# Kernel tuning notes

Measured on AMD Instinct MI355X. Metric: run time of the kernel, lower is better.

Reference implementation:

```python
import jax, jax.numpy as jnp
import numpy as np

E, B = 4, 16384
STATE, ACT, HID = 29, 8, 512
N_POSE, N_LEG = 13, 16

def _leg_inputs(state, act=None):
    # gather per-leg features: for each leg i (stride-2 over 8 joints)
    # [pos_a, vel_a, pos_b, vel_b, (act_a, act_b)] -> concat legs along batch dim
    leg = state[..., -N_LEG:]
    blocks = []
    for i in range(0, 8, 2):
        feats = [leg[..., i], leg[..., 8 + i], leg[..., i + 1], leg[..., 8 + i + 1]]
        if act is not None:
            feats += [act[..., i], act[..., i + 1]]
        blocks.append(jnp.stack(feats, axis=2))
    return jnp.concatenate(blocks, axis=1)  # [E, 4B, 4 or 6]

def _mlp(x, w0, b0, w1, b1, w2, b2, mu, sigma):
    x = (x - mu) / (sigma + 1e-8)
    x = jax.nn.relu(jnp.einsum('ebi,eih->ebh', x, w0) + b0)
    x = jax.nn.relu(jnp.einsum('ebh,ehk->ebk', x, w1) + b1)
    return jnp.einsum('ebh,eho->ebo', x, w2) + b2

def _leg_format(next_legs, b):
    # vectorized form of the original nested-loop scatter in leg_predict
    e = next_legs.shape[0]
    c = next_legs.reshape(e, 4, b, 4).transpose(0, 2, 1, 3)  # [E,B,leg,comp]
    first = jnp.stack([c[..., 0], c[..., 2]], axis=-1).reshape(e, b, 8)   # pos block
    second = jnp.stack([c[..., 1], c[..., 3]], axis=-1).reshape(e, b, 8)  # vel block
    zeros = jnp.zeros((e, b, N_POSE), next_legs.dtype)
    return jnp.concatenate([zeros, first, second], axis=-1)  # [E,B,29]

def reference(state, act, wl0, bl0, wl1, bl1, wl2, bl2, wp0, bp0, wp1, bp1, wp2, bp2,
              mu_leg, sigma_leg, mu_pose, sigma_pose,
              mu_t_leg, sigma_t_leg, mu_t_pose, sigma_t_pose):
    b = state.shape[1]
    out = _mlp(_leg_inputs(state, act), wl0, bl0, wl1, bl1, wl2, bl2, mu_leg, sigma_leg)
    legs_diff = out[..., :4] * (sigma_t_leg + 1e-8) + mu_t_leg          # [E,4B,4] mean head
    legs_curr = _leg_inputs(state)                                       # [E,4B,4]
    next_state_legs = _leg_format(legs_curr + legs_diff, b)              # [E,B,29]
    legs_diff_fmt = _leg_format(legs_diff, b)[..., -N_LEG:]              # [E,B,16]
    pose_in = jnp.concatenate([state[..., :N_POSE], legs_diff_fmt], axis=-1)  # [E,B,29]
    pose = _mlp(pose_in, wp0, bp0, wp1, bp1, wp2, bp2, mu_pose, sigma_pose)[..., :N_POSE]
    pose = pose * (sigma_t_pose + 1e-8) + mu_t_pose + state[..., :N_POSE]
    next_state = jnp.concatenate([pose, next_state_legs[..., N_POSE:]], axis=-1)
    return next_state.mean(0)  # [B, 29]

def setup_inputs():
    key = jax.random.key(0)
    ks = jax.random.split(key, 10)
    s = 0.05
    return {
        'state': jax.random.normal(ks[0], (E, B, STATE), jnp.float32),
        'act': jax.random.normal(ks[1], (E, B, ACT), jnp.float32),
        'wl0': jax.random.normal(ks[2], (E, 6, HID), jnp.float32) * s,
        'bl0': jnp.zeros((E, 1, HID), jnp.float32),
        'wl1': jax.random.normal(ks[3], (E, HID, HID), jnp.float32) * s,
        'bl1': jnp.zeros((E, 1, HID), jnp.float32),
        'wl2': jax.random.normal(ks[4], (E, HID, 8), jnp.float32) * s,
        'bl2': jnp.zeros((E, 1, 8), jnp.float32),
        'wp0': jax.random.normal(ks[5], (E, STATE, HID), jnp.float32) * s,
        'bp0': jnp.zeros((E, 1, HID), jnp.float32),
        'wp1': jax.random.normal(ks[6], (E, HID, HID), jnp.float32) * s,
        'bp1': jnp.zeros((E, 1, HID), jnp.float32),
        'wp2': jax.random.normal(ks[7], (E, HID, 2 * N_POSE), jnp.float32) * s,
        'bp2': jnp.zeros((E, 1, 2 * N_POSE), jnp.float32),
        'mu_leg': jnp.zeros((1, 6), jnp.float32),
        'sigma_leg': jnp.ones((1, 6), jnp.float32),
        'mu_pose': jnp.zeros((1, STATE), jnp.float32),
        'sigma_pose': jnp.ones((1, STATE), jnp.float32),
        'mu_t_leg': jnp.zeros((1, 4), jnp.float32),
        'sigma_t_leg': jnp.ones((1, 4), jnp.float32),
        'mu_t_pose': jnp.zeros((1, N_POSE), jnp.float32),
        'sigma_t_pose': jnp.ones((1, N_POSE), jnp.float32),
    }
```

## Files before the change

### kernel.cpp

```cpp
#include <hip/hip_runtime.h>


#define E_ 4
#define B_ 16384
#define H1S 520
#define H2S 136
#define A0S 40

typedef float f32x4 __attribute__((ext_vector_type(4)));
typedef __bf16 bf16x8 __attribute__((ext_vector_type(8)));

__device__ __forceinline__ f32x4 mfma16(bf16x8 a, bf16x8 b, f32x4 c) {
  return __builtin_amdgcn_mfma_f32_16x16x32_bf16(a, b, c, 0, 0, 0);
}

__device__ __forceinline__ void fmt_map(int k, int& ib, int& j) {
  if (k < 8) { ib = k >> 1; j = (k & 1) ? 2 : 0; }
  else { int k8 = k - 8; ib = k8 >> 1; j = (k8 & 1) ? 3 : 1; }
}

__device__ __forceinline__ void pack_one(int idx, int per_e, int KT, int Kreal,
                                         int Nsrc, int Nval,
                                         const float* __restrict__ src,
                                         const float* __restrict__ sigma,
                                         __bf16* __restrict__ dst)
{
  int e = idx / per_e;
  int rem = idx - e * per_e;
  int g = rem >> 9;
  int nt = g / KT;
  int kt = g - nt * KT;
  int li = rem & 511;
  int lane = li >> 3, j = li & 7;
  int k = kt * 32 + (lane >> 4) * 8 + j;
  int n = nt * 16 + (lane & 15);
  float v = 0.f;
  if (k < Kreal && n < Nval) {
    v = src[(size_t)e * Kreal * Nsrc + (size_t)k * Nsrc + n];
    if (sigma) v *= 1.f / (sigma[k] + 1e-8f);
  }
  dst[idx] = (__bf16)v;
}

__global__ void prep_kernel(const float* __restrict__ wl0, const float* __restrict__ wl1,
                            const float* __restrict__ wl2, const float* __restrict__ wp0,
                            const float* __restrict__ wp1, const float* __restrict__ wp2,
                            const float* __restrict__ bl0, const float* __restrict__ bp0,
                            const float* __restrict__ mu_leg, const float* __restrict__ sigma_leg,
                            const float* __restrict__ mu_pose, const float* __restrict__ sigma_pose,
                            __bf16* __restrict__ WL0p, __bf16* __restrict__ WL1p,
                            __bf16* __restrict__ WL2p, __bf16* __restrict__ WP0p,
                            __bf16* __restrict__ WP1p, __bf16* __restrict__ WP2p,
                            float* __restrict__ bl0f, float* __restrict__ bp0f)
{
  const int S0 = 65536, S1 = 1048576, S2 = 32768;
  const int total = 2 * (S0 + S1 + S2) + 4096;
  for (int idx0 = blockIdx.x * blockDim.x + threadIdx.x; idx0 < total;
       idx0 += gridDim.x * blockDim.x) {
    int x = idx0;
    if (x < S0)              { pack_one(x, 16384, 1, 6, 512, 512, wl0, sigma_leg, WL0p); }
    else if ((x -= S0) < S1) { pack_one(x, 262144, 16, 512, 512, 512, wl1, nullptr, WL1p); }
    else if ((x -= S1) < S2) { pack_one(x, 8192, 16, 512, 8, 8, wl2, nullptr, WL2p); }
    else if ((x -= S2) < S0) { pack_one(x, 16384, 1, 29, 512, 512, wp0, sigma_pose, WP0p); }
    else if ((x -= S0) < S1) { pack_one(x, 262144, 16, 512, 512, 512, wp1, nullptr, WP1p); }
    else if ((x -= S1) < S2) { pack_one(x, 8192, 16, 512, 26, 16, wp2, nullptr, WP2p); }
    else {
      x -= S2;
      if (x < 2048) {
        int e = x >> 9, n = x & 511;
        float s = bl0[e * 512 + n];
        #pragma unroll
        for (int k = 0; k < 6; ++k)
          s -= mu_leg[k] / (sigma_leg[k] + 1e-8f) * wl0[(e * 6 + k) * 512 + n];
        bl0f[e * 512 + n] = s;
      } else {
        x -= 2048;
        int e = x >> 9, n = x & 511;
        float s = bp0[e * 512 + n];
        for (int k = 0; k < 29; ++k)
          s -= mu_pose[k] / (sigma_pose[k] + 1e-8f) * wp0[(e * 29 + k) * 512 + n];
        bp0f[e * 512 + n] = s;
      }
    }
  }
}

__global__ __launch_bounds__(512) void fused_kernel(
    const float* __restrict__ state, const float* __restrict__ act,
    const float* __restrict__ bl1, const float* __restrict__ bl2,
    const float* __restrict__ bp1, const float* __restrict__ bp2,
    const float* __restrict__ mu_t_leg, const float* __restrict__ sigma_t_leg,
    const float* __restrict__ mu_t_pose, const float* __restrict__ sigma_t_pose,
    const __bf16* __restrict__ WL0p, const __bf16* __restrict__ WL1p,
    const __bf16* __restrict__ WL2p, const __bf16* __restrict__ WP0p,
    const __bf16* __restrict__ WP1p, const __bf16* __restrict__ WP2p,
    const float* __restrict__ bl0f, const float* __restrict__ bp0f,
    float* __restrict__ out)
{
  __shared__ alignas(16) __bf16 h1[128 * H1S];
  __shared__ alignas(16) __bf16 h2c[64 * H2S];
  __shared__ float ldiff[64][16];
  __shared__ float legacc[64][16];
  __bf16* a0s = h2c;

  const int tid = threadIdx.x;
  const int wv = tid >> 6;
  const int lane = tid & 63;
  const int quad = lane >> 4;
  const int l16 = lane & 15;
  const int b0 = blockIdx.x * 64;

  for (int i = tid; i < 64 * 16; i += 512) ((float*)legacc)[i] = 0.f;
  f32x4 posacc = {0.f, 0.f, 0.f, 0.f};
  __syncthreads();

  for (int e = 0; e < E_; ++e) {
    const float* se = state + (size_t)e * B_ * 29;
    const float* ae = act + (size_t)e * B_ * 8;

    for (int half = 0; half < 2; ++half) {
      __syncthreads();
      for (int i = tid; i < 128 * 32; i += 512) {
        int r = i >> 5, c = i & 31;
        float v = 0.f;
        if (c < 6) {
          int ib = r >> 5;
          int b = b0 + half * 32 + (r & 31);
          const float* sp = se + (size_t)b * 29;
          if (c == 0) v = sp[13 + 2 * ib];
          else if (c == 1) v = sp[21 + 2 * ib];
          else if (c == 2) v = sp[14 + 2 * ib];
          else if (c == 3) v = sp[22 + 2 * ib];
          else if (c == 4) v = ae[(size_t)b * 8 + 2 * ib];
          else v = ae[(size_t)b * 8 + 2 * ib + 1];
        }
        a0s[r * A0S + c] = (__bf16)v;
      }
      __syncthreads();

      {
        const __bf16* W0 = WL0p + (size_t)e * 16384;
        const float* b0v = bl0f + e * 512;
        bf16x8 bfr[4]; float bs[4];
        #pragma unroll
        for (int i = 0; i < 4; ++i) {
          int ct = wv * 4 + i;
          bfr[i] = *(const bf16x8*)(W0 + ((size_t)ct * 64 + lane) * 8);
          bs[i] = b0v[ct * 16 + l16];
        }
        for (int rt = 0; rt < 8; ++rt) {
          bf16x8 afr = *(const bf16x8*)&a0s[(rt * 16 + l16) * A0S + quad * 8];
          #pragma unroll
          for (int i = 0; i < 4; ++i) {
            f32x4 acc = {bs[i], bs[i], bs[i], bs[i]};
            acc = mfma16(afr, bfr[i], acc);
            int col = (wv * 4 + i) * 16 + l16;
            #pragma unroll
            for (int r = 0; r < 4; ++r)
              h1[(rt * 16 + quad * 4 + r) * H1S + col] = (__bf16)fmaxf(acc[r], 0.f);
          }
        }
      }
      __syncthreads();

      const __bf16* W1 = WL1p + (size_t)e * 262144;
      const __bf16* W2 = WL2p + (size_t)e * 8192;
      const float* b1v = bl1 + e * 512;
      const int rg = wv >> 2, cg = wv & 3;
      float bv2 = (l16 < 8) ? bl2[e * 8 + l16] : 0.f;
      f32x4 oacc = {bv2, bv2, bv2, bv2};

      for (int cc = 0; cc < 4; ++cc) {
        f32x4 acc[4][2];
        #pragma unroll
        for (int ct = 0; ct < 2; ++ct) {
          float bias = b1v[cc * 128 + cg * 32 + ct * 16 + l16];
          #pragma unroll
          for (int i = 0; i < 4; ++i) acc[i][ct] = (f32x4){bias, bias, bias, bias};
        }
        const __bf16* Wc = W1 + (size_t)(cc * 8 + cg * 2) * 8192;
        #pragma unroll 4
        for (int kt = 0; kt < 16; ++kt) {
          bf16x8 afr[4];
          #pragma unroll
          for (int i = 0; i < 4; ++i)
            afr[i] = *(const bf16x8*)&h1[(rg * 64 + i * 16 + l16) * H1S + kt * 32 + quad * 8];
          #pragma unroll
          for (int ct = 0; ct < 2; ++ct) {
            bf16x8 bfr = *(const bf16x8*)(Wc + (((size_t)ct * 16 + kt) * 64 + lane) * 8);
            #pragma unroll
            for (int i = 0; i < 4; ++i) acc[i][ct] = mfma16(afr[i], bfr, acc[i][ct]);
          }
        }
        #pragma unroll
        for (int hh = 0; hh < 2; ++hh) {
          __syncthreads();
          if (rg == hh) {
            #pragma unroll
            for (int i = 0; i < 4; ++i)
              #pragma unroll
              for (int ct = 0; ct < 2; ++ct)
                #pragma unroll
                for (int r = 0; r < 4; ++r)
                  h2c[(i * 16 + quad * 4 + r) * H2S + cg * 32 + ct * 16 + l16] =
                      (__bf16)fmaxf(acc[i][ct][r], 0.f);
          }
          __syncthreads();
          if ((wv >> 2) == hh) {
            #pragma unroll
            for (int k2 = 0; k2 < 4; ++k2) {
              bf16x8 afr2 = *(const bf16x8*)&h2c[((wv & 3) * 16 + l16) * H2S + k2 * 32 + quad * 8];
              bf16x8 bfr2 = *(const bf16x8*)(W2 + ((size_t)(cc * 4 + k2) * 64 + lane) * 8);
              oacc = mfma16(afr2, bfr2, oacc);
            }
          }
        }
      }
      if (l16 < 4) {
        float sc = sigma_t_leg[l16] + 1e-8f;
        float mv = mu_t_leg[l16];
        #pragma unroll
        for (int r = 0; r < 4; ++r) {
          int L = wv * 16 + quad * 4 + r;
          ldiff[half * 32 + (L & 31)][(L >> 5) * 4 + l16] = oacc[r] * sc + mv;
        }
      }
    }

    __syncthreads();
    for (int i = tid; i < 64 * 32; i += 512) {
      int t = i >> 5, c = i & 31;
      float v = 0.f;
      if (c < 13) v = se[(size_t)(b0 + t) * 29 + c];
      else if (c < 29) { int ib, j; fmt_map(c - 13, ib, j); v = ldiff[t][ib * 4 + j]; }
      a0s[t * A0S + c] = (__bf16)v;
    }
    for (int i = tid; i < 64 * 16; i += 512) {
      int t = i >> 4, k = i & 15;
      int ib, j; fmt_map(k, ib, j);
      legacc[t][k] += se[(size_t)(b0 + t) * 29 + 13 + k] + ldiff[t][ib * 4 + j];
    }
    __syncthreads();

    {
      const __bf16* W0 = WP0p + (size_t)e * 16384;
      const float* b0v = bp0f + e * 512;
      bf16x8 bfr[4]; float bs[4];
      #pragma unroll
      for (int i = 0; i < 4; ++i) {
        int ct = wv * 4 + i;
        bfr[i] = *(const bf16x8*)(W0 + ((size_t)ct * 64 + lane) * 8);
        bs[i] = b0v[ct * 16 + l16];
      }
      for (int rt = 0; rt < 4; ++rt) {
        bf16x8 afr = *(const bf16x8*)&a0s[(rt * 16 + l16) * A0S + quad * 8];
        #pragma unroll
        for (int i = 0; i < 4; ++i) {
          f32x4 acc = {bs[i], bs[i], bs[i], bs[i]};
          acc = mfma16(afr, bfr[i], acc);
          int col = (wv * 4 + i) * 16 + l16;
          #pragma unroll
          for (int r = 0; r < 4; ++r)
            h1[(rt * 16 + quad * 4 + r) * H1S + col] = (__bf16)fmaxf(acc[r], 0.f);
        }
      }
    }
    __syncthreads();

    {
      const __bf16* W1 = WP1p + (size_t)e * 262144;
      const __bf16* W2 = WP2p + (size_t)e * 8192;
      const float* b1v = bp1 + e * 512;
      float bvp = bp2[e * 26 + l16];
      f32x4 po = {bvp, bvp, bvp, bvp};

      for (int cc2 = 0; cc2 < 2; ++cc2) {
        f32x4 acc[4][2];
        #pragma unroll
        for (int ct = 0; ct < 2; ++ct) {
          float bias = b1v[cc2 * 256 + wv * 32 + ct * 16 + l16];
          #pragma unroll
          for (int i = 0; i < 4; ++i) acc[i][ct] = (f32x4){bias, bias, bias, bias};
        }
        const __bf16* Wc = W1 + (size_t)(cc2 * 16 + wv * 2) * 8192;
        #pragma unroll 4
        for (int kt = 0; kt < 16; ++kt) {
          bf16x8 afr[4];
          #pragma unroll
          for (int i = 0; i < 4; ++i)
            afr[i] = *(const bf16x8*)&h1[(i * 16 + l16) * H1S + kt * 32 + quad * 8];
          #pragma unroll
          for (int ct = 0; ct < 2; ++ct) {
            bf16x8 bfr = *(const bf16x8*)(Wc + (((size_t)ct * 16 + kt) * 64 + lane) * 8);
            #pragma unroll
            for (int i = 0; i < 4; ++i) acc[i][ct] = mfma16(afr[i], bfr, acc[i][ct]);
          }
        }
        #pragma unroll
        for (int hh = 0; hh < 2; ++hh) {
          __syncthreads();
          if ((wv >> 2) == hh) {
            int cgl = wv & 3;
            #pragma unroll
            for (int i = 0; i < 4; ++i)
              #pragma unroll
              for (int ct = 0; ct < 2; ++ct)
                #pragma unroll
                for (int r = 0; r < 4; ++r)
                  h2c[(i * 16 + quad * 4 + r) * H2S + cgl * 32 + ct * 16 + l16] =
                      (__bf16)fmaxf(acc[i][ct][r], 0.f);
          }
          __syncthreads();
          if (wv < 4) {
            #pragma unroll
            for (int k2 = 0; k2 < 4; ++k2) {
              bf16x8 afr2 = *(const bf16x8*)&h2c[(wv * 16 + l16) * H2S + k2 * 32 + quad * 8];
              bf16x8 bfr2 = *(const bf16x8*)(W2 + ((size_t)(cc2 * 8 + hh * 4 + k2) * 64 + lane) * 8);
              po = mfma16(afr2, bfr2, po);
            }
          }
        }
      }
      if (wv < 4 && l16 < 13) {
        float sc = sigma_t_pose[l16] + 1e-8f;
        float mv = mu_t_pose[l16];
        #pragma unroll
        for (int r = 0; r < 4; ++r) {
          int row = wv * 16 + quad * 4 + r;
          posacc[r] += po[r] * sc + mv + se[(size_t)(b0 + row) * 29 + l16];
        }
      }
    }
  }

  if (wv < 4 && l16 < 13) {
    #pragma unroll
    for (int r = 0; r < 4; ++r) {
      int row = wv * 16 + quad * 4 + r;
      out[(size_t)(b0 + row) * 29 + l16] = 0.25f * posacc[r];
    }
  }
  for (int i = tid; i < 64 * 16; i += 512) {
    int t = i >> 4, k = i & 15;
    out[(size_t)(b0 + t) * 29 + 13 + k] = 0.25f * legacc[t][k];
  }
}

extern "C" void kernel_launch(void* const* d_in, const int* in_sizes, int n_in,
                              void* d_out, int out_size, void* d_ws, size_t ws_size,
                              hipStream_t stream) {
  const float* state = (const float*)d_in[0];
  const float* act = (const float*)d_in[1];
  const float* wl0 = (const float*)d_in[2];
  const float* bl0 = (const float*)d_in[3];
  const float* wl1 = (const float*)d_in[4];
  const float* bl1 = (const float*)d_in[5];
  const float* wl2 = (const float*)d_in[6];
  const float* bl2 = (const float*)d_in[7];
  const float* wp0 = (const float*)d_in[8];
  const float* bp0 = (const float*)d_in[9];
  const float* wp1 = (const float*)d_in[10];
  const float* bp1 = (const float*)d_in[11];
  const float* wp2 = (const float*)d_in[12];
  const float* bp2 = (const float*)d_in[13];
  const float* mu_leg = (const float*)d_in[14];
  const float* sigma_leg = (const float*)d_in[15];
  const float* mu_pose = (const float*)d_in[16];
  const float* sigma_pose = (const float*)d_in[17];
  const float* mu_t_leg = (const float*)d_in[18];
  const float* sigma_t_leg = (const float*)d_in[19];
  const float* mu_t_pose = (const float*)d_in[20];
  const float* sigma_t_pose = (const float*)d_in[21];
  float* out = (float*)d_out;

  char* ws = (char*)d_ws;
  __bf16* WL0p = (__bf16*)(ws);
  __bf16* WL1p = (__bf16*)(ws + 131072);
  __bf16* WL2p = (__bf16*)(ws + 2228224);
  __bf16* WP0p = (__bf16*)(ws + 2293760);
  __bf16* WP1p = (__bf16*)(ws + 2424832);
  __bf16* WP2p = (__bf16*)(ws + 4521984);
  float* bl0f = (float*)(ws + 4587520);
  float* bp0f = (float*)(ws + 4595712);

  prep_kernel<<<512, 256, 0, stream>>>(wl0, wl1, wl2, wp0, wp1, wp2, bl0, bp0,
                                       mu_leg, sigma_leg, mu_pose, sigma_pose,
                                       WL0p, WL1p, WL2p, WP0p, WP1p, WP2p,
                                       bl0f, bp0f);
  fused_kernel<<<256, 512, 0, stream>>>(state, act, bl1, bl2, bp1, bp2,
                                        mu_t_leg, sigma_t_leg, mu_t_pose, sigma_t_pose,
                                        WL0p, WL1p, WL2p, WP0p, WP1p, WP2p,
                                        bl0f, bp0f, out);
}
```

Baseline: 375.7 us.

## Halve block tile to 32 rows, 256 threads, XOR-swizzled LDS without padding

Each block now handles 32 batch rows with 4 waves instead of 64 rows with 8 waves, and the grid doubles to 512 blocks. Launch bounds ask for two blocks per CU so more work is resident. Padded LDS strides give way to an XOR swizzle on the h1/h2 buffers, which shrinks LDS use while still avoiding bank conflicts. Leg accumulators move into registers, and the pose-head partial sums are reduced across waves through LDS. The cost is that each block reloads the weights for half as many rows, so weight traffic per row doubles, and there are more barriers.

```diff
diff --git a/kernel.cpp b/kernel.cpp
--- a/kernel.cpp
+++ b/kernel.cpp
@@ -3,15 +3,19 @@
 
 #define E_ 4
 #define B_ 16384
-#define H1S 520
-#define H2S 136
-#define A0S 40
 
 typedef float f32x4 __attribute__((ext_vector_type(4)));
 typedef __bf16 bf16x8 __attribute__((ext_vector_type(8)));
 
 __device__ __forceinline__ f32x4 mfma16(bf16x8 a, bf16x8 b, f32x4 c) {
   return __builtin_amdgcn_mfma_f32_16x16x32_bf16(a, b, c, 0, 0, 0);
+}
+
+__device__ __forceinline__ __bf16* swz_ptr(__bf16* base, int row, int col,
+                                           int rowshift) {
+  int byte = (row << rowshift) + (col << 1);
+  byte ^= (row & 7) << 4;
+  return (__bf16*)((char*)base + byte);
 }
 
 __device__ __forceinline__ void fmt_map(int k, int& ib, int& j) {
@@ -85,7 +89,7 @@
   }
 }
 
-__global__ __launch_bounds__(512) void fused_kernel(
+__global__ __launch_bounds__(256, 2) void fused_kernel(
     const float* __restrict__ state, const float* __restrict__ act,
     const float* __restrict__ bl1, const float* __restrict__ bl2,
     const float* __restrict__ bp1, const float* __restrict__ bp2,
@@ -97,10 +101,9 @@
     const float* __restrict__ bl0f, const float* __restrict__ bp0f,
     float* __restrict__ out)
 {
-  __shared__ alignas(16) __bf16 h1[128 * H1S];
-  __shared__ alignas(16) __bf16 h2c[64 * H2S];
-  __shared__ float ldiff[64][16];
-  __shared__ float legacc[64][16];
+  __shared__ alignas(16) __bf16 h1[64 * 512];
+  __shared__ alignas(16) __bf16 h2c[64 * 64];
+  __shared__ float ldiff[32][16];
   __bf16* a0s = h2c;
 
   const int tid = threadIdx.x;
@@ -108,56 +111,56 @@
   const int lane = tid & 63;
   const int quad = lane >> 4;
   const int l16 = lane & 15;
-  const int b0 = blockIdx.x * 64;
-
-  for (int i = tid; i < 64 * 16; i += 512) ((float*)legacc)[i] = 0.f;
+  const int b0 = blockIdx.x * 32;
+
+  const int lt = tid >> 3;
+  const int lk = tid & 7;
+  float legacc0 = 0.f, legacc1 = 0.f;
   f32x4 posacc = {0.f, 0.f, 0.f, 0.f};
-  __syncthreads();
 
   for (int e = 0; e < E_; ++e) {
     const float* se = state + (size_t)e * B_ * 29;
     const float* ae = act + (size_t)e * B_ * 8;
 
-    for (int half = 0; half < 2; ++half) {
+    for (int h = 0; h < 2; ++h) {
       __syncthreads();
-      for (int i = tid; i < 128 * 32; i += 512) {
+      for (int i = tid; i < 64 * 32; i += 256) {
         int r = i >> 5, c = i & 31;
+        int ib = h * 2 + (r >> 5);
+        int b = b0 + (r & 31);
+        const float* sp = se + (size_t)b * 29;
         float v = 0.f;
-        if (c < 6) {
-          int ib = r >> 5;
-          int b = b0 + half * 32 + (r & 31);
-          const float* sp = se + (size_t)b * 29;
-          if (c == 0) v = sp[13 + 2 * ib];
-          else if (c == 1) v = sp[21 + 2 * ib];
-          else if (c == 2) v = sp[14 + 2 * ib];
-          else if (c == 3) v = sp[22 + 2 * ib];
-          else if (c == 4) v = ae[(size_t)b * 8 + 2 * ib];
-          else v = ae[(size_t)b * 8 + 2 * ib + 1];
-        }
-        a0s[r * A0S + c] = (__bf16)v;
+        if (c == 0) v = sp[13 + 2 * ib];
+        else if (c == 1) v = sp[21 + 2 * ib];
+        else if (c == 2) v = sp[14 + 2 * ib];
+        else if (c == 3) v = sp[22 + 2 * ib];
+        else if (c == 4) v = ae[(size_t)b * 8 + 2 * ib];
+        else if (c == 5) v = ae[(size_t)b * 8 + 2 * ib + 1];
+        a0s[r * 40 + c] = (__bf16)v;
       }
       __syncthreads();
 
       {
         const __bf16* W0 = WL0p + (size_t)e * 16384;
         const float* b0v = bl0f + e * 512;
-        bf16x8 bfr[4]; float bs[4];
-        #pragma unroll
-        for (int i = 0; i < 4; ++i) {
-          int ct = wv * 4 + i;
+        bf16x8 bfr[8]; float bs[8];
+        #pragma unroll
+        for (int i = 0; i < 8; ++i) {
+          int ct = wv * 8 + i;
           bfr[i] = *(const bf16x8*)(W0 + ((size_t)ct * 64 + lane) * 8);
           bs[i] = b0v[ct * 16 + l16];
         }
-        for (int rt = 0; rt < 8; ++rt) {
-          bf16x8 afr = *(const bf16x8*)&a0s[(rt * 16 + l16) * A0S + quad * 8];
-          #pragma unroll
-          for (int i = 0; i < 4; ++i) {
+        for (int rt = 0; rt < 4; ++rt) {
+          bf16x8 afr = *(const bf16x8*)&a0s[(rt * 16 + l16) * 40 + quad * 8];
+          #pragma unroll
+          for (int i = 0; i < 8; ++i) {
             f32x4 acc = {bs[i], bs[i], bs[i], bs[i]};
             acc = mfma16(afr, bfr[i], acc);
-            int col = (wv * 4 + i) * 16 + l16;
+            int col = (wv * 8 + i) * 16 + l16;
             #pragma unroll
             for (int r = 0; r < 4; ++r)
-              h1[(rt * 16 + quad * 4 + r) * H1S + col] = (__bf16)fmaxf(acc[r], 0.f);
+              *swz_ptr(h1, rt * 16 + quad * 4 + r, col, 10) =
+                  (__bf16)fmaxf(acc[r], 0.f);
           }
         }
       }
@@ -166,53 +169,48 @@
       const __bf16* W1 = WL1p + (size_t)e * 262144;
       const __bf16* W2 = WL2p + (size_t)e * 8192;
       const float* b1v = bl1 + e * 512;
-      const int rg = wv >> 2, cg = wv & 3;
       float bv2 = (l16 < 8) ? bl2[e * 8 + l16] : 0.f;
       f32x4 oacc = {bv2, bv2, bv2, bv2};
 
-      for (int cc = 0; cc < 4; ++cc) {
-        f32x4 acc[4][2];
-        #pragma unroll
-        for (int ct = 0; ct < 2; ++ct) {
-          float bias = b1v[cc * 128 + cg * 32 + ct * 16 + l16];
-          #pragma unroll
-          for (int i = 0; i < 4; ++i) acc[i][ct] = (f32x4){bias, bias, bias, bias};
-        }
-        const __bf16* Wc = W1 + (size_t)(cc * 8 + cg * 2) * 8192;
+      for (int cc = 0; cc < 2; ++cc) {
+        f32x4 acc[4][4];
+        #pragma unroll
+        for (int ctw = 0; ctw < 4; ++ctw) {
+          float bias = b1v[cc * 256 + ctw * 64 + wv * 16 + l16];
+          #pragma unroll
+          for (int i = 0; i < 4; ++i) acc[i][ctw] = (f32x4){bias, bias, bias, bias};
+        }
         #pragma unroll 4
         for (int kt = 0; kt < 16; ++kt) {
           bf16x8 afr[4];
           #pragma unroll
           for (int i = 0; i < 4; ++i)
-            afr[i] = *(const bf16x8*)&h1[(rg * 64 + i * 16 + l16) * H1S + kt * 32 + quad * 8];
-          #pragma unroll
-          for (int ct = 0; ct < 2; ++ct) {
-            bf16x8 bfr = *(const bf16x8*)(Wc + (((size_t)ct * 16 + kt) * 64 + lane) * 8);
+            afr[i] = *(const bf16x8*)swz_ptr(h1, i * 16 + l16,
+                                             kt * 32 + quad * 8, 10);
+          #pragma unroll
+          for (int ctw = 0; ctw < 4; ++ctw) {
+            int nt = cc * 16 + ctw * 4 + wv;
+            bf16x8 bfr = *(const bf16x8*)(W1 + (((size_t)nt * 16 + kt) * 64 + lane) * 8);
             #pragma unroll
-            for (int i = 0; i < 4; ++i) acc[i][ct] = mfma16(afr[i], bfr, acc[i][ct]);
-          }
-        }
-        #pragma unroll
-        for (int hh = 0; hh < 2; ++hh) {
+            for (int i = 0; i < 4; ++i) acc[i][ctw] = mfma16(afr[i], bfr, acc[i][ctw]);
+          }
+        }
+        #pragma unroll
+        for (int ctw = 0; ctw < 4; ++ctw) {
           __syncthreads();
-          if (rg == hh) {
+          #pragma unroll
+          for (int i = 0; i < 4; ++i)
             #pragma unroll
-            for (int i = 0; i < 4; ++i)
-              #pragma unroll
-              for (int ct = 0; ct < 2; ++ct)
-                #pragma unroll
-                for (int r = 0; r < 4; ++r)
-                  h2c[(i * 16 + quad * 4 + r) * H2S + cg * 32 + ct * 16 + l16] =
-                      (__bf16)fmaxf(acc[i][ct][r], 0.f);
-          }
+            for (int r = 0; r < 4; ++r)
+              *swz_ptr(h2c, i * 16 + quad * 4 + r, wv * 16 + l16, 7) =
+                  (__bf16)fmaxf(acc[i][ctw][r], 0.f);
           __syncthreads();
-          if ((wv >> 2) == hh) {
-            #pragma unroll
-            for (int k2 = 0; k2 < 4; ++k2) {
-              bf16x8 afr2 = *(const bf16x8*)&h2c[((wv & 3) * 16 + l16) * H2S + k2 * 32 + quad * 8];
-              bf16x8 bfr2 = *(const bf16x8*)(W2 + ((size_t)(cc * 4 + k2) * 64 + lane) * 8);
-              oacc = mfma16(afr2, bfr2, oacc);
-            }
+          #pragma unroll
+          for (int k2 = 0; k2 < 2; ++k2) {
+            bf16x8 afr2 = *(const bf16x8*)swz_ptr(h2c, wv * 16 + l16,
+                                                  k2 * 32 + quad * 8, 7);
+            bf16x8 bfr2 = *(const bf16x8*)(W2 + ((size_t)((cc * 8 + ctw * 2 + k2) * 64 + lane)) * 8);
+            oacc = mfma16(afr2, bfr2, oacc);
           }
         }
       }
@@ -222,46 +220,49 @@
         #pragma unroll
         for (int r = 0; r < 4; ++r) {
           int L = wv * 16 + quad * 4 + r;
-          ldiff[half * 32 + (L & 31)][(L >> 5) * 4 + l16] = oacc[r] * sc + mv;
+          int ib = h * 2 + (L >> 5);
+          ldiff[L & 31][ib * 4 + l16] = oacc[r] * sc + mv;
         }
       }
     }
 
     __syncthreads();
-    for (int i = tid; i < 64 * 32; i += 512) {
+    for (int i = tid; i < 32 * 32; i += 256) {
       int t = i >> 5, c = i & 31;
       float v = 0.f;
       if (c < 13) v = se[(size_t)(b0 + t) * 29 + c];
       else if (c < 29) { int ib, j; fmt_map(c - 13, ib, j); v = ldiff[t][ib * 4 + j]; }
-      a0s[t * A0S + c] = (__bf16)v;
-    }
-    for (int i = tid; i < 64 * 16; i += 512) {
-      int t = i >> 4, k = i & 15;
-      int ib, j; fmt_map(k, ib, j);
-      legacc[t][k] += se[(size_t)(b0 + t) * 29 + 13 + k] + ldiff[t][ib * 4 + j];
+      a0s[t * 40 + c] = (__bf16)v;
+    }
+    {
+      int ib0, j0, ib1, j1;
+      fmt_map(lk, ib0, j0); fmt_map(lk + 8, ib1, j1);
+      legacc0 += se[(size_t)(b0 + lt) * 29 + 13 + lk] + ldiff[lt][ib0 * 4 + j0];
+      legacc1 += se[(size_t)(b0 + lt) * 29 + 21 + lk] + ldiff[lt][ib1 * 4 + j1];
     }
     __syncthreads();
 
     {
       const __bf16* W0 = WP0p + (size_t)e * 16384;
       const float* b0v = bp0f + e * 512;
-      bf16x8 bfr[4]; float bs[4];
+      bf16x8 bfr[8]; float bs[8];
       #pragma unroll
-      for (int i = 0; i < 4; ++i) {
-        int ct = wv * 4 + i;
+      for (int i = 0; i < 8; ++i) {
+        int ct = wv * 8 + i;
         bfr[i] = *(const bf16x8*)(W0 + ((size_t)ct * 64 + lane) * 8);
         bs[i] = b0v[ct * 16 + l16];
       }
-      for (int rt = 0; rt < 4; ++rt) {
-        bf16x8 afr = *(const bf16x8*)&a0s[(rt * 16 + l16) * A0S + quad * 8];
-        #pragma unroll
-        for (int i = 0; i < 4; ++i) {
+      for (int rt = 0; rt < 2; ++rt) {
+        bf16x8 afr = *(const bf16x8*)&a0s[(rt * 16 + l16) * 40 + quad * 8];
+        #pragma unroll
+        for (int i = 0; i < 8; ++i) {
           f32x4 acc = {bs[i], bs[i], bs[i], bs[i]};
           acc = mfma16(afr, bfr[i], acc);
-          int col = (wv * 4 + i) * 16 + l16;
+          int col = (wv * 8 + i) * 16 + l16;
           #pragma unroll
           for (int r = 0; r < 4; ++r)
-            h1[(rt * 16 + quad * 4 + r) * H1S + col] = (__bf16)fmaxf(acc[r], 0.f);
+            *swz_ptr(h1, rt * 16 + quad * 4 + r, col, 10) =
+                (__bf16)fmaxf(acc[r], 0.f);
         }
       }
     }
@@ -271,79 +272,87 @@
       const __bf16* W1 = WP1p + (size_t)e * 262144;
       const __bf16* W2 = WP2p + (size_t)e * 8192;
       const float* b1v = bp1 + e * 512;
-      float bvp = bp2[e * 26 + l16];
+      float bvp = (wv < 2) ? bp2[e * 26 + l16] : 0.f;
       f32x4 po = {bvp, bvp, bvp, bvp};
 
-      for (int cc2 = 0; cc2 < 2; ++cc2) {
-        f32x4 acc[4][2];
-        #pragma unroll
-        for (int ct = 0; ct < 2; ++ct) {
-          float bias = b1v[cc2 * 256 + wv * 32 + ct * 16 + l16];
-          #pragma unroll
-          for (int i = 0; i < 4; ++i) acc[i][ct] = (f32x4){bias, bias, bias, bias};
-        }
-        const __bf16* Wc = W1 + (size_t)(cc2 * 16 + wv * 2) * 8192;
+      for (int cc = 0; cc < 2; ++cc) {
+        f32x4 acc[2][4];
+        #pragma unroll
+        for (int ctw = 0; ctw < 4; ++ctw) {
+          float bias = b1v[cc * 256 + ctw * 64 + wv * 16 + l16];
+          #pragma unroll
+          for (int i = 0; i < 2; ++i) acc[i][ctw] = (f32x4){bias, bias, bias, bias};
+        }
         #pragma unroll 4
         for (int kt = 0; kt < 16; ++kt) {
-          bf16x8 afr[4];
-          #pragma unroll
-          for (int i = 0; i < 4; ++i)
-            afr[i] = *(const bf16x8*)&h1[(i * 16 + l16) * H1S + kt * 32 + quad * 8];
-          #pragma unroll
-          for (int ct = 0; ct < 2; ++ct) {
-            bf16x8 bfr = *(const bf16x8*)(Wc + (((size_t)ct * 16 + kt) * 64 + lane) * 8);
+          bf16x8 afr[2];
+          #pragma unroll
+          for (int i = 0; i < 2; ++i)
+            afr[i] = *(const bf16x8*)swz_ptr(h1, i * 16 + l16,
+                                             kt * 32 + quad * 8, 10);
+          #pragma unroll
+          for (int ctw = 0; ctw < 4; ++ctw) {
+            int nt = cc * 16 + ctw * 4 + wv;
+            bf16x8 bfr = *(const bf16x8*)(W1 + (((size_t)nt * 16 + kt) * 64 + lane) * 8);
             #pragma unroll
-            for (int i = 0; i < 4; ++i) acc[i][ct] = mfma16(afr[i], bfr, acc[i][ct]);
-          }
-        }
-        #pragma unroll
-        for (int hh = 0; hh < 2; ++hh) {
+            for (int i = 0; i < 2; ++i) acc[i][ctw] = mfma16(afr[i], bfr, acc[i][ctw]);
+          }
+        }
+        #pragma unroll
+        for (int sp = 0; sp < 2; ++sp) {
           __syncthreads();
-          if ((wv >> 2) == hh) {
-            int cgl = wv & 3;
+          #pragma unroll
+          for (int cw = 0; cw < 2; ++cw) {
+            int ctw = sp * 2 + cw;
             #pragma unroll
-            for (int i = 0; i < 4; ++i)
+            for (int i = 0; i < 2; ++i)
               #pragma unroll
-              for (int ct = 0; ct < 2; ++ct)
-                #pragma unroll
-                for (int r = 0; r < 4; ++r)
-                  h2c[(i * 16 + quad * 4 + r) * H2S + cgl * 32 + ct * 16 + l16] =
-                      (__bf16)fmaxf(acc[i][ct][r], 0.f);
+              for (int r = 0; r < 4; ++r)
+                *swz_ptr(h2c, i * 16 + quad * 4 + r, cw * 64 + wv * 16 + l16, 8) =
+                    (__bf16)fmaxf(acc[i][ctw][r], 0.f);
           }
           __syncthreads();
-          if (wv < 4) {
-            #pragma unroll
-            for (int k2 = 0; k2 < 4; ++k2) {
-              bf16x8 afr2 = *(const bf16x8*)&h2c[(wv * 16 + l16) * H2S + k2 * 32 + quad * 8];
-              bf16x8 bfr2 = *(const bf16x8*)(W2 + ((size_t)(cc2 * 8 + hh * 4 + k2) * 64 + lane) * 8);
-              po = mfma16(afr2, bfr2, po);
-            }
-          }
-        }
-      }
-      if (wv < 4 && l16 < 13) {
+          #pragma unroll
+          for (int kk = 0; kk < 2; ++kk) {
+            int k2 = (wv >> 1) * 2 + kk;
+            bf16x8 afr2 = *(const bf16x8*)swz_ptr(h2c, (wv & 1) * 16 + l16,
+                                                  k2 * 32 + quad * 8, 8);
+            int k2g = cc * 8 + sp * 4 + k2;
+            bf16x8 bfr2 = *(const bf16x8*)(W2 + ((size_t)(k2g * 64 + lane)) * 8);
+            po = mfma16(afr2, bfr2, po);
+          }
+        }
+      }
+      __syncthreads();
+      float* pored = (float*)h2c;
+      if (wv >= 2) {
+        #pragma unroll
+        for (int r = 0; r < 4; ++r)
+          pored[((wv & 1) * 16 + quad * 4 + r) * 16 + l16] = po[r];
+      }
+      __syncthreads();
+      if (wv < 2 && l16 < 13) {
         float sc = sigma_t_pose[l16] + 1e-8f;
         float mv = mu_t_pose[l16];
         #pragma unroll
         for (int r = 0; r < 4; ++r) {
           int row = wv * 16 + quad * 4 + r;
-          posacc[r] += po[r] * sc + mv + se[(size_t)(b0 + row) * 29 + l16];
+          float tot = po[r] + pored[row * 16 + l16];
+          posacc[r] += tot * sc + mv + se[(size_t)(b0 + row) * 29 + l16];
         }
       }
     }
   }
 
-  if (wv < 4 && l16 < 13) {
+  if (wv < 2 && l16 < 13) {
     #pragma unroll
     for (int r = 0; r < 4; ++r) {
       int row = wv * 16 + quad * 4 + r;
       out[(size_t)(b0 + row) * 29 + l16] = 0.25f * posacc[r];
     }
   }
-  for (int i = tid; i < 64 * 16; i += 512) {
-    int t = i >> 4, k = i & 15;
-    out[(size_t)(b0 + t) * 29 + 13 + k] = 0.25f * legacc[t][k];
-  }
+  out[(size_t)(b0 + lt) * 29 + 13 + lk] = 0.25f * legacc0;
+  out[(size_t)(b0 + lt) * 29 + 21 + lk] = 0.25f * legacc1;
 }
 
 extern "C" void kernel_launch(void* const* d_in, const int* in_sizes, int n_in,
@@ -387,7 +396,7 @@
                                        mu_leg, sigma_leg, mu_pose, sigma_pose,
                                        WL0p, WL1p, WL2p, WP0p, WP1p, WP2p,
                                        bl0f, bp0f);
-  fused_kernel<<<256, 512, 0, stream>>>(state, act, bl1, bl2, bp1, bp2,
+  fused_kernel<<<512, 256, 0, stream>>>(state, act, bl1, bl2, bp1, bp2,
                                         mu_t_leg, sigma_t_leg, mu_t_pose, sigma_t_pose,
                                         WL0p, WL1p, WL2p, WP0p, WP1p, WP2p,
                                         bl0f, bp0f, out);
```

After: 854.1 us. +127.3%, slower.

## Swizzle LDS activation buffers and transpose-pack hidden weights through shared memory

Applied to the files above, without the earlier changes.

Replaces the padded row strides of the h1/h2c shared-memory activation buffers with an XOR swizzle on 16-byte chunks, so the bf16x8 MFMA operand reads avoid bank conflicts without padding. Splits the weight-packing prep into a small kernel and a dedicated kernel for the two 512x512 hidden matrices. That kernel reads float4 rows coalesced, stages them in LDS, and writes packed bf16x8 fragments, replacing the strided per-element gathers. This adds a kernel launch, and the swizzled scalar writes into h1 may still conflict.

```diff
diff --git a/kernel.cpp b/kernel.cpp
--- a/kernel.cpp
+++ b/kernel.cpp
@@ -3,8 +3,6 @@
 
 #define E_ 4
 #define B_ 16384
-#define H1S 520
-#define H2S 136
 #define A0S 40
 
 typedef float f32x4 __attribute__((ext_vector_type(4)));
@@ -12,6 +10,17 @@
 
 __device__ __forceinline__ f32x4 mfma16(bf16x8 a, bf16x8 b, f32x4 c) {
   return __builtin_amdgcn_mfma_f32_16x16x32_bf16(a, b, c, 0, 0, 0);
+}
+
+__device__ __forceinline__ __bf16* swzh1(__bf16* base, int row, int col) {
+  int byte = (row << 10) + (col << 1);
+  byte ^= (row & 7) << 4;
+  return (__bf16*)((char*)base + byte);
+}
+__device__ __forceinline__ __bf16* swzh2(__bf16* base, int row, int col) {
+  int byte = (row << 8) + (col << 1);
+  byte ^= (row & 7) << 4;
+  return (__bf16*)((char*)base + byte);
 }
 
 __device__ __forceinline__ void fmt_map(int k, int& ib, int& j) {
@@ -42,28 +51,24 @@
   dst[idx] = (__bf16)v;
 }
 
-__global__ void prep_kernel(const float* __restrict__ wl0, const float* __restrict__ wl1,
-                            const float* __restrict__ wl2, const float* __restrict__ wp0,
-                            const float* __restrict__ wp1, const float* __restrict__ wp2,
-                            const float* __restrict__ bl0, const float* __restrict__ bp0,
-                            const float* __restrict__ mu_leg, const float* __restrict__ sigma_leg,
-                            const float* __restrict__ mu_pose, const float* __restrict__ sigma_pose,
-                            __bf16* __restrict__ WL0p, __bf16* __restrict__ WL1p,
-                            __bf16* __restrict__ WL2p, __bf16* __restrict__ WP0p,
-                            __bf16* __restrict__ WP1p, __bf16* __restrict__ WP2p,
-                            float* __restrict__ bl0f, float* __restrict__ bp0f)
+__global__ void prep_small(const float* __restrict__ wl0, const float* __restrict__ wl2,
+                           const float* __restrict__ wp0, const float* __restrict__ wp2,
+                           const float* __restrict__ bl0, const float* __restrict__ bp0,
+                           const float* __restrict__ mu_leg, const float* __restrict__ sigma_leg,
+                           const float* __restrict__ mu_pose, const float* __restrict__ sigma_pose,
+                           __bf16* __restrict__ WL0p, __bf16* __restrict__ WL2p,
+                           __bf16* __restrict__ WP0p, __bf16* __restrict__ WP2p,
+                           float* __restrict__ bl0f, float* __restrict__ bp0f)
 {
-  const int S0 = 65536, S1 = 1048576, S2 = 32768;
-  const int total = 2 * (S0 + S1 + S2) + 4096;
+  const int S0 = 65536, S2 = 32768;
+  const int total = 2 * (S0 + S2) + 4096;
   for (int idx0 = blockIdx.x * blockDim.x + threadIdx.x; idx0 < total;
        idx0 += gridDim.x * blockDim.x) {
     int x = idx0;
     if (x < S0)              { pack_one(x, 16384, 1, 6, 512, 512, wl0, sigma_leg, WL0p); }
-    else if ((x -= S0) < S1) { pack_one(x, 262144, 16, 512, 512, 512, wl1, nullptr, WL1p); }
-    else if ((x -= S1) < S2) { pack_one(x, 8192, 16, 512, 8, 8, wl2, nullptr, WL2p); }
+    else if ((x -= S0) < S2) { pack_one(x, 8192, 16, 512, 8, 8, wl2, nullptr, WL2p); }
     else if ((x -= S2) < S0) { pack_one(x, 16384, 1, 29, 512, 512, wp0, sigma_pose, WP0p); }
-    else if ((x -= S0) < S1) { pack_one(x, 262144, 16, 512, 512, 512, wp1, nullptr, WP1p); }
-    else if ((x -= S1) < S2) { pack_one(x, 8192, 16, 512, 26, 16, wp2, nullptr, WP2p); }
+    else if ((x -= S0) < S2) { pack_one(x, 8192, 16, 512, 26, 16, wp2, nullptr, WP2p); }
     else {
       x -= S2;
       if (x < 2048) {
@@ -82,6 +87,42 @@
         bp0f[e * 512 + n] = s;
       }
     }
+  }
+}
+
+__global__ __launch_bounds__(256) void prep_w1(const float* __restrict__ wl1,
+                                               const float* __restrict__ wp1,
+                                               __bf16* __restrict__ WL1p,
+                                               __bf16* __restrict__ WP1p)
+{
+  __shared__ __bf16 st[512][20];
+  const int b = blockIdx.x;
+  const float* src = (b & 128) ? wp1 : wl1;
+  __bf16* dst = (b & 128) ? WP1p : WL1p;
+  const int e = (b >> 5) & 3, nt = b & 31;
+  src += (size_t)e * 262144 + nt * 16;
+  dst += (size_t)e * 262144 + (size_t)nt * 8192;
+  const int t = threadIdx.x;
+
+  const int k0 = t >> 2, nq = t & 3;
+  #pragma unroll
+  for (int it = 0; it < 8; ++it) {
+    int k = it * 64 + k0;
+    f32x4 v = *(const f32x4*)(src + (size_t)k * 512 + nq * 4);
+    #pragma unroll
+    for (int j = 0; j < 4; ++j) st[k][nq * 4 + j] = (__bf16)v[j];
+  }
+  __syncthreads();
+  #pragma unroll
+  for (int it = 0; it < 4; ++it) {
+    int lo = it * 256 + t;
+    int kt = lo >> 6, lane = lo & 63;
+    int kb = kt * 32 + (lane >> 4) * 8;
+    int n = lane & 15;
+    bf16x8 o;
+    #pragma unroll
+    for (int j = 0; j < 8; ++j) o[j] = st[kb + j][n];
+    *(bf16x8*)(dst + (size_t)lo * 8) = o;
   }
 }
 
@@ -97,8 +138,8 @@
     const float* __restrict__ bl0f, const float* __restrict__ bp0f,
     float* __restrict__ out)
 {
-  __shared__ alignas(16) __bf16 h1[128 * H1S];
-  __shared__ alignas(16) __bf16 h2c[64 * H2S];
+  __shared__ alignas(16) __bf16 h1[128 * 512];
+  __shared__ alignas(16) __bf16 h2c[64 * 128];
   __shared__ float ldiff[64][16];
   __shared__ float legacc[64][16];
   __bf16* a0s = h2c;
@@ -157,7 +198,7 @@
             int col = (wv * 4 + i) * 16 + l16;
             #pragma unroll
             for (int r = 0; r < 4; ++r)
-              h1[(rt * 16 + quad * 4 + r) * H1S + col] = (__bf16)fmaxf(acc[r], 0.f);
+              *swzh1(h1, rt * 16 + quad * 4 + r, col) = (__bf16)fmaxf(acc[r], 0.f);
           }
         }
       }
@@ -184,7 +225,8 @@
           bf16x8 afr[4];
           #pragma unroll
           for (int i = 0; i < 4; ++i)
-            afr[i] = *(const bf16x8*)&h1[(rg * 64 + i * 16 + l16) * H1S + kt * 32 + quad * 8];
+            afr[i] = *(const bf16x8*)swzh1(h1, rg * 64 + i * 16 + l16,
+                                           kt * 32 + quad * 8);
           #pragma unroll
           for (int ct = 0; ct < 2; ++ct) {
             bf16x8 bfr = *(const bf16x8*)(Wc + (((size_t)ct * 16 + kt) * 64 + lane) * 8);
@@ -202,14 +244,15 @@
               for (int ct = 0; ct < 2; ++ct)
                 #pragma unroll
                 for (int r = 0; r < 4; ++r)
-                  h2c[(i * 16 + quad * 4 + r) * H2S + cg * 32 + ct * 16 + l16] =
+                  *swzh2(h2c, i * 16 + quad * 4 + r, cg * 32 + ct * 16 + l16) =
                       (__bf16)fmaxf(acc[i][ct][r], 0.f);
           }
           __syncthreads();
           if ((wv >> 2) == hh) {
             #pragma unroll
             for (int k2 = 0; k2 < 4; ++k2) {
-              bf16x8 afr2 = *(const bf16x8*)&h2c[((wv & 3) * 16 + l16) * H2S + k2 * 32 + quad * 8];
+              bf16x8 afr2 = *(const bf16x8*)swzh2(h2c, (wv & 3) * 16 + l16,
+                                                  k2 * 32 + quad * 8);
               bf16x8 bfr2 = *(const bf16x8*)(W2 + ((size_t)(cc * 4 + k2) * 64 + lane) * 8);
               oacc = mfma16(afr2, bfr2, oacc);
             }
@@ -261,7 +304,7 @@
           int col = (wv * 4 + i) * 16 + l16;
           #pragma unroll
           for (int r = 0; r < 4; ++r)
-            h1[(rt * 16 + quad * 4 + r) * H1S + col] = (__bf16)fmaxf(acc[r], 0.f);
+            *swzh1(h1, rt * 16 + quad * 4 + r, col) = (__bf16)fmaxf(acc[r], 0.f);
         }
       }
     }
@@ -288,7 +331,7 @@
           bf16x8 afr[4];
           #pragma unroll
           for (int i = 0; i < 4; ++i)
-            afr[i] = *(const bf16x8*)&h1[(i * 16 + l16) * H1S + kt * 32 + quad * 8];
+            afr[i] = *(const bf16x8*)swzh1(h1, i * 16 + l16, kt * 32 + quad * 8);
           #pragma unroll
           for (int ct = 0; ct < 2; ++ct) {
             bf16x8 bfr = *(const bf16x8*)(Wc + (((size_t)ct * 16 + kt) * 64 + lane) * 8);
@@ -307,14 +350,15 @@
               for (int ct = 0; ct < 2; ++ct)
                 #pragma unroll
                 for (int r = 0; r < 4; ++r)
-                  h2c[(i * 16 + quad * 4 + r) * H2S + cgl * 32 + ct * 16 + l16] =
+                  *swzh2(h2c, i * 16 + quad * 4 + r, cgl * 32 + ct * 16 + l16) =
                       (__bf16)fmaxf(acc[i][ct][r], 0.f);
           }
           __syncthreads();
           if (wv < 4) {
             #pragma unroll
             for (int k2 = 0; k2 < 4; ++k2) {
-              bf16x8 afr2 = *(const bf16x8*)&h2c[(wv * 16 + l16) * H2S + k2 * 32 + quad * 8];
+              bf16x8 afr2 = *(const bf16x8*)swzh2(h2c, wv * 16 + l16,
+                                                  k2 * 32 + quad * 8);
               bf16x8 bfr2 = *(const bf16x8*)(W2 + ((size_t)(cc2 * 8 + hh * 4 + k2) * 64 + lane) * 8);
               po = mfma16(afr2, bfr2, po);
             }
@@ -383,10 +427,10 @@
   float* bl0f = (float*)(ws + 4587520);
   float* bp0f = (float*)(ws + 4595712);
 
-  prep_kernel<<<512, 256, 0, stream>>>(wl0, wl1, wl2, wp0, wp1, wp2, bl0, bp0,
-                                       mu_leg, sigma_leg, mu_pose, sigma_pose,
-                                       WL0p, WL1p, WL2p, WP0p, WP1p, WP2p,
-                                       bl0f, bp0f);
+  prep_small<<<256, 256, 0, stream>>>(wl0, wl2, wp0, wp2, bl0, bp0,
+                                      mu_leg, sigma_leg, mu_pose, sigma_pose,
+                                      WL0p, WL2p, WP0p, WP2p, bl0f, bp0f);
+  prep_w1<<<256, 256, 0, stream>>>(wl1, wp1, WL1p, WP1p);
   fused_kernel<<<256, 512, 0, stream>>>(state, act, bl1, bl2, bp1, bp2,
                                         mu_t_leg, sigma_t_leg, mu_t_pose, sigma_t_pose,
                                         WL0p, WL1p, WL2p, WP0p, WP1p, WP2p,
```

Result: slower. 588.0 us (+56.5%).
